# Optimization experiments

Hardware: AMD Instinct MI355X
Metric: run time of the kernel (lower is better)

Reference implementation:

```python
import jax, jax.numpy as jnp
import numpy as np
import math

D_MODEL = 1024
N_HEADS = 16
HEAD_DIM = D_MODEL // N_HEADS
B, S = 4, 4096


def setup_inputs() -> dict:
    key = jax.random.key(0)
    ks = jax.random.split(key, 8)
    # xavier-uniform-ish scale for square DxD matrices
    lim = math.sqrt(6.0 / (D_MODEL + D_MODEL))
    def W(k):
        return jax.random.uniform(k, (D_MODEL, D_MODEL), jnp.float32, -lim, lim)
    return {
        "x": jax.random.normal(ks[0], (B, S, D_MODEL), jnp.float32),
        "fractal_dim": jnp.float32(1.7),
        "Wq": W(ks[1]), "bq": jnp.zeros((D_MODEL,), jnp.float32),
        "Wk": W(ks[2]), "bk": jnp.zeros((D_MODEL,), jnp.float32),
        "Wv": W(ks[3]), "bv": jnp.zeros((D_MODEL,), jnp.float32),
        "Wo": W(ks[4]), "bo": jnp.zeros((D_MODEL,), jnp.float32),
        "alpha": jnp.float32(1.5),
        "frac_scale": jnp.float32(0.5),
    }


def reference(x, fractal_dim, Wq, bq, Wk, bk, Wv, bv, Wo, bo, alpha, frac_scale):
    b, s, d = x.shape
    h, hd = N_HEADS, HEAD_DIM
    residual = x

    adaptive_alpha = alpha + frac_scale * (fractal_dim - 1.5)

    q = (x @ Wq + bq).reshape(b, s, h, hd)
    k = (x @ Wk + bk).reshape(b, s, h, hd)
    v = (x @ Wv + bv).reshape(b, s, h, hd)

    # spectral filter over frequency axis (seq dim)
    freqs = jnp.fft.fftfreq(s).astype(x.dtype)  # [S]
    phase = adaptive_alpha * jnp.arctan(jnp.log(jnp.abs(freqs) + 1e-10))
    filt = jnp.exp(1j * phase)[None, :, None, None]  # [1,S,1,1] complex

    def spectral(t):
        tf = jnp.fft.fft(t, axis=1, norm="ortho") * filt
        return jnp.fft.ifft(tf, axis=1, norm="ortho").real

    q_t, k_t, v_t = spectral(q), spectral(k), spectral(v)

    # per-(token) dot product across head_dim -> logits over heads
    logits = jnp.einsum("bshd,bshd->bsh", q_t, k_t) / math.sqrt(hd)
    w = jax.nn.softmax(logits, axis=-1)  # softmax over heads
    attended = w[..., None] * v_t  # [B,S,H,Hd]

    # final inverse FFT of the (real) attended signal along seq dim
    attended_time = jnp.fft.ifft(attended.astype(jnp.complex64), axis=1, norm="ortho").real

    out = attended_time.reshape(b, s, d) @ Wo + bo
    return out + residual
```

## Files before the change

kernel.cpp:

```cpp
#include <hip/hip_runtime.h>

#define S      4096
#define DM     1024
#define NB     4
#define NH     16
#define HDIM   64
#define MTOT   (NB * S)
#define DS     ((long)DM * S)
#define MH     2304
#define KH     2112
#define KH2    2112
#define MEO    2048

typedef __attribute__((ext_vector_type(8))) short short8;
typedef __attribute__((ext_vector_type(4))) float f32x4;
typedef __attribute__((ext_vector_type(8))) unsigned short u16x8;
typedef __attribute__((ext_vector_type(4))) unsigned short u16x4;

__device__ __forceinline__ unsigned short f2bf(float f) {
  union { float f; unsigned u; } v; v.f = f;
  unsigned r = v.u + 0x7fffu + ((v.u >> 16) & 1u);
  return (unsigned short)(r >> 16);
}
__device__ __forceinline__ float bf2f(short h) {
  union { unsigned u; float f; } v; v.u = ((unsigned)(unsigned short)h) << 16;
  return v.f;
}

#define GLOAD(gp, lp) __builtin_amdgcn_global_load_lds( \
    (const __attribute__((address_space(1))) void*)(gp), \
    (__attribute__((address_space(3))) void*)(lp), 16, 0, 0)

#define SBAR() do { asm volatile("" ::: "memory"); __builtin_amdgcn_s_barrier(); \
                    asm volatile("" ::: "memory"); } while (0)
#define WAITL0() asm volatile("s_waitcnt lgkmcnt(0)" ::: "memory")

#define SWZ(o) ((o) ^ ((((o) >> 7) & 3) << 4))


__global__ void k_tabg(const float* __restrict__ fd, const float* __restrict__ alpha,
                       const float* __restrict__ fsc,
                       float* __restrict__ cos_tab, float* __restrict__ c_arr,
                       float* __restrict__ g) {
  const float twopi = 6.28318530717958647692f;
  float aa = alpha[0] + fsc[0] * (fd[0] - 1.5f);
  int bx = blockIdx.x;
  if (bx < 16) {
    int k = bx * 256 + threadIdx.x;
    cos_tab[k] = cosf(twopi * ((float)k / (float)S));
    int kk = (k <= S / 2) ? k : (S - k);
    float af = (float)kk / (float)S;
    c_arr[k] = cosf(aa * atanf(logf(af + 1e-10f)));
    return;
  }
  __shared__ float sct[S];
  __shared__ float sc[S];
  __shared__ float red[16][17];
  for (int i = threadIdx.x; i < S; i += 256) {
    sct[i] = cosf(twopi * ((float)i / (float)S));
    int kk = (i <= S / 2) ? i : (S - i);
    float af = (float)kk / (float)S;
    sc[i] = cosf(aa * atanf(logf(af + 1e-10f)));
  }
  __syncthreads();
  int jl = threadIdx.x >> 4, r = threadIdx.x & 15;
  int j = (bx - 16) * 16 + jl;
  float acc = 0.f;
#pragma unroll 4
  for (int i = 0; i < 256; ++i) {
    int k = r + 16 * i;
    acc += sc[k] * sct[(j * k) & (S - 1)];
  }
  red[jl][r] = acc;
  __syncthreads();
  if (r == 0) {
    float s = 0.f;
#pragma unroll
    for (int i = 0; i < 16; ++i) s += red[jl][i];
    g[j] = s * (1.f / (float)S);
  }
}

__global__ void k_buildEO(const float* __restrict__ g, short* __restrict__ Ge) {
  long i8 = ((long)blockIdx.x * 256 + threadIdx.x) * 8;
  if (i8 >= (long)MEO * KH2) return;
  int n = (int)(i8 / KH2);
  int m = (int)(i8 % KH2);
  u16x8 ev, ov;
#pragma unroll
  for (int j = 0; j < 8; ++j) {
    int mm = m + j;
    float e, o;
    if (mm == 0)            { e = g[n]; o = 0.f; }
    else if (mm == 2048)    { e = g[(n + 2048) & (S - 1)]; o = 0.f; }
    else if (mm > 2048)     { e = 0.f; o = 0.f; }
    else {
      float a = g[(n - mm) & (S - 1)], b = g[(n + mm) & (S - 1)];
      e = 0.5f * (a + b); o = 0.5f * (a - b);
    }
    ev[j] = f2bf(e); ov[j] = f2bf(o);
  }
  *(u16x8*)(Ge + i8) = ev;
  *(u16x8*)(Ge + (long)MEO * KH2 + i8) = ov;
}

__global__ void k_prep(const float* __restrict__ x, short* __restrict__ uv,
                       const float* __restrict__ W0, const float* __restrict__ W1,
                       const float* __restrict__ W2, const float* __restrict__ W3,
                       short* __restrict__ WT) {
  __shared__ float sh[2 * 64 * 65];
  int bx = blockIdx.x, by = blockIdx.y, bz = blockIdx.z;
  int t = threadIdx.x;
  int r = t >> 4, c4 = (t & 15) * 4;
  if (bx >= 33) {
    float (*tile)[65] = (float(*)[65])sh;
    const float* W = (bz == 0) ? W0 : ((bz == 1) ? W1 : ((bz == 2) ? W2 : W3));
    short* WTo = WT + (size_t)bz * DM * DM;
    int k0 = (bx - 33) * 64, n0 = by * 64;
    const float* ip = W + (long)k0 * DM + n0;
#pragma unroll
    for (int rr = 0; rr < 4; ++rr) {
      float4 v = *(const float4*)(ip + (long)(r + rr * 16) * DM + c4);
      tile[r + rr * 16][c4 + 0] = v.x;
      tile[r + rr * 16][c4 + 1] = v.y;
      tile[r + rr * 16][c4 + 2] = v.z;
      tile[r + rr * 16][c4 + 3] = v.w;
    }
    __syncthreads();
    int k_loc = t & 63, nq = t >> 6;
    short* op = WTo + (long)n0 * DM + k0;
#pragma unroll
    for (int i = 0; i < 16; ++i) {
      int n_loc = nq * 16 + i;
      op[(long)n_loc * DM + k_loc] = (short)f2bf(tile[k_loc][n_loc]);
    }
    return;
  }
  float (*tp)[65] = (float(*)[65])sh;
  float (*tm)[65] = (float(*)[65])(sh + 64 * 65);
  int m0 = bx * 64, d0 = by * 64, b = bz;
#pragma unroll
  for (int rr = 0; rr < 4; ++rr) {
    int m = m0 + r + rr * 16;
    float4 vp = *(const float4*)(x + ((long)(b * S + m)) * DM + d0 + c4);
    int ms = (S - m) & (S - 1);
    float4 vm = *(const float4*)(x + ((long)(b * S + ms)) * DM + d0 + c4);
    tp[r + rr * 16][c4 + 0] = vp.x; tp[r + rr * 16][c4 + 1] = vp.y;
    tp[r + rr * 16][c4 + 2] = vp.z; tp[r + rr * 16][c4 + 3] = vp.w;
    tm[r + rr * 16][c4 + 0] = vm.x; tm[r + rr * 16][c4 + 1] = vm.y;
    tm[r + rr * 16][c4 + 2] = vm.z; tm[r + rr * 16][c4 + 3] = vm.w;
  }
  __syncthreads();
  int m_loc = t & 63, dq = t >> 6;
#pragma unroll
  for (int i = 0; i < 16; ++i) {
    int d_loc = dq * 16 + i;
    int m = m0 + m_loc;
    float P = tp[m_loc][d_loc], M = tm[m_loc][d_loc];
    float u, v;
    if (m == 0 || m == 2048) { u = P; v = 0.f; }
    else if (m > 2048)       { u = 0.f; v = 0.f; }
    else                     { u = P + M; v = P - M; }
    long base = ((long)(b * DM + d0 + d_loc)) * KH2 + m;
    uv[base] = (short)f2bf(u);
    uv[base + (long)4 * DM * KH2] = (short)f2bf(v);
  }
}

__global__ void k_unfold2(const short* __restrict__ AB, const float* __restrict__ g,
                          const short* __restrict__ uv, short* __restrict__ Xs) {
  __shared__ float red[256];
  int bx = blockIdx.x;
  if (bx < 4096) {
    long i8 = ((long)bx * 256 + threadIdx.x) * 8;
    int b = (int)(i8 >> 21);
    long rr = i8 & ((1L << 21) - 1);
    int n = (int)(rr >> 10);
    int d = (int)(rr & (DM - 1));
    u16x8 av = *(const u16x8*)(AB + i8);
    u16x8 bv = *(const u16x8*)(AB + ((long)4 * MEO * DM) + i8);
    u16x8 sv, dv;
#pragma unroll
    for (int j = 0; j < 8; ++j) {
      float A = bf2f((short)av[j]), B = bf2f((short)bv[j]);
      sv[j] = f2bf(A + B);
      dv[j] = f2bf(A - B);
    }
    *(u16x8*)(Xs + ((long)b * S + n) * DM + d) = sv;
    if (n > 0)
      *(u16x8*)(Xs + ((long)b * S + (S - n)) * DM + d) = dv;
  } else {
    int bd = bx - 4096;
    int b = bd >> 10, d = bd & (DM - 1);
    const short* up = uv + ((long)(b * DM + d)) * KH2;
    int t = threadIdx.x;
    float acc = 0.f;
    for (int m = t; m <= 2048; m += 256)
      acc += g[2048 - m] * bf2f(up[m]);
    red[t] = acc;
    __syncthreads();
    for (int sh = 128; sh > 0; sh >>= 1) {
      if (t < sh) red[t] += red[t + sh];
      __syncthreads();
    }
    if (t == 0) Xs[((long)b * S + 2048) * DM + d] = (short)f2bf(red[0]);
  }
}

__global__ void k_logsoft(const short* __restrict__ Q, const short* __restrict__ K,
                          float* __restrict__ w) {
  int idx = blockIdx.x * 16 + (threadIdx.x >> 4);
  int h = threadIdx.x & 15;
  const short* q = Q + (long)idx * DM + h * HDIM;
  const short* k = K + (long)idx * DM + h * HDIM;
  float acc = 0.f;
#pragma unroll
  for (int jj = 0; jj < 8; ++jj) {
    u16x8 qa = *(const u16x8*)(q + jj * 8);
    u16x8 ka = *(const u16x8*)(k + jj * 8);
#pragma unroll
    for (int l = 0; l < 8; ++l) acc += bf2f((short)qa[l]) * bf2f((short)ka[l]);
  }
  acc *= 0.125f;
  float m = acc;
#pragma unroll
  for (int d = 1; d < 16; d <<= 1) m = fmaxf(m, __shfl_xor(m, d, 16));
  float e = expf(acc - m);
  float ssum = e;
#pragma unroll
  for (int d = 1; d < 16; d <<= 1) ssum += __shfl_xor(ssum, d, 16);
  int b = idx >> 12, s = idx & (S - 1);
  w[((long)b * NH + h) * S + s] = e / ssum;
}

__global__ void k_attfoldM2(const short* __restrict__ V, const float* __restrict__ wsm,
                            short* __restrict__ A2t,
                            const float* __restrict__ cos_tab, short* __restrict__ Mc2) {
  int bx = blockIdx.x, by = blockIdx.y, bz = blockIdx.z;
  if (bx >= 33) {
    long lin = (long)(bx - 33) + 38L * (by + 16L * bz);
    long i8 = (lin * 256 + threadIdx.x) * 8;
    if (i8 >= (long)MH * KH) return;
    int n = (int)(i8 / KH);
    int m = (int)(i8 % KH);
    u16x8 mv;
#pragma unroll
    for (int j = 0; j < 8; ++j) {
      int mm = m + j;
      float vv = (mm <= 2048) ? cos_tab[(n * mm) & (S - 1)] * 0.015625f : 0.f;
      mv[j] = f2bf(vv);
    }
    *(u16x8*)(Mc2 + i8) = mv;
    return;
  }
  __shared__ float t1[64][65];
  __shared__ float t2[64][65];
  __shared__ float w1[64], w2[64];
  int m0 = bx * 64, d0 = by * 64, b = bz;
  int t = threadIdx.x;
  int h0 = d0 >> 6;
  if (t < 64) {
    int m = m0 + t;
    const float* wp = wsm + ((long)b * NH + h0) * S;
    w1[t] = wp[m & (S - 1)];
    w2[t] = wp[(S - m) & (S - 1)];
  }
  int r = t >> 4, c4 = (t & 15) * 4;
#pragma unroll
  for (int rr = 0; rr < 4; ++rr) {
    int i = r + rr * 16;
    int m = m0 + i;
    u16x4 a = *(const u16x4*)(V + ((long)(b * S + (m & (S - 1)))) * DM + d0 + c4);
    u16x4 bb = *(const u16x4*)(V + ((long)(b * S + ((S - m) & (S - 1)))) * DM + d0 + c4);
#pragma unroll
    for (int l = 0; l < 4; ++l) {
      t1[i][c4 + l] = bf2f((short)a[l]);
      t2[i][c4 + l] = bf2f((short)bb[l]);
    }
  }
  __syncthreads();
  int i_loc = t & 63, jq = t >> 6;
  int m = m0 + i_loc;
#pragma unroll
  for (int jj = 0; jj < 16; ++jj) {
    int j = jq * 16 + jj;
    float rv;
    if (m == 0 || m == 2048) rv = w1[i_loc] * t1[i_loc][j];
    else if (m < 2048)       rv = w1[i_loc] * t1[i_loc][j] + w2[i_loc] * t2[i_loc][j];
    else                     rv = 0.f;
    A2t[((long)(b * DM + d0 + j)) * KH + m] = (short)f2bf(rv);
  }
}

template <int EPI, int AMIR = 0, int ASEL = 0, int WALK = 0, int MREP = 1>
__global__ __launch_bounds__(512, 2) void gemm8(
    const short* __restrict__ A, const short* __restrict__ Bt,
    short* __restrict__ Cb, short* __restrict__ Cb2, short* __restrict__ Cb3,
    float* __restrict__ Cf,
    const float* __restrict__ bias, const float* __restrict__ bias2,
    const float* __restrict__ bias3,
    const float* __restrict__ bsc, const float* __restrict__ resid,
    int M, int N, int K, long aBatch, long bBatch, long cBatch) {
  __shared__ __align__(16) short SH[65536];
  auto Ab = [&](int buf, int ks) { return SH + (buf * 2 + ks) * 8192; };
  auto Bb = [&](int buf, int ks) { return SH + 32768 + (buf * 2 + ks) * 8192; };

  const int gx = gridDim.x, gy = gridDim.y;
  const int nwg = gx * gy * gridDim.z;
  int lin = blockIdx.x + gx * (blockIdx.y + gy * blockIdx.z);
  int swz = lin;
  if ((nwg & 7) == 0) {
    const int cpx = nwg >> 3;
    swz = (lin & 7) * cpx + (lin >> 3);
  }
  const int NTN = N >> 8;
  const int NTM = M >> 8;
  const int tid = threadIdx.x;
  const int lane = tid & 63;
  const int wid = tid >> 6;
  const int wm = wid >> 2, wn = wid & 3;

  const int o0 = tid * 16, o1 = o0 + 8192;
  const int lo0 = SWZ(o0), lo1 = SWZ(o1);
  const int srow[2] = {lo0 >> 6, lo1 >> 6};
  const int scol[2] = {(lo0 & 63) >> 1, (lo1 & 63) >> 1};

  for (int rep = 0; rep < MREP; ++rep) {
    const int wg = swz + rep * nwg;
    int ntile, mtile, bz;
    if (WALK) {
      mtile = wg % NTM;
      const int rest = wg / NTM;
      ntile = rest % NTN;
      bz = rest / NTN;
    } else {
      ntile = wg % NTN;
      const int rest = wg / NTN;
      mtile = rest % NTM;
      bz = rest / NTM;
    }

    const short* Ag = ASEL ? (A + (long)(bz >> 2) * aBatch) : (A + (long)bz * aBatch);
    const short* Bg = Bt + (long)bz * bBatch;
    const int m0 = mtile << 8, n0 = ntile << 8;

    const short* bA[2];
    const short* bB[2];
#pragma unroll
    for (int j = 0; j < 2; ++j) {
      if (AMIR) {
        int grow = m0 + srow[j];
        int b_ = grow >> 12, s_ = grow & (S - 1);
        int sm = (s_ <= 2048) ? s_ : (4096 - s_);
        bA[j] = Ag + ((long)b_ * MH + sm) * K + scol[j];
      } else {
        bA[j] = Ag + (long)(m0 + srow[j]) * K + scol[j];
      }
      bB[j] = Bg + (long)(n0 + srow[j]) * K + scol[j];
    }

    f32x4 acc[8][4];
#pragma unroll
    for (int i = 0; i < 8; ++i)
#pragma unroll
      for (int j = 0; j < 4; ++j) acc[i][j] = (f32x4){0.f, 0.f, 0.f, 0.f};

    const int NT = K >> 6;
    auto stage = [&](int h) {
      const int tau = h >> 2, q = h & 3;
      const int ks = q >> 1;
      const long k0 = (long)tau * 64 + ks * 32;
      const int dbase = (q & 1) * 65536 + (((tau & 1) << 1) + ks) * 16384;
      const short* b0 = (q & 1) ? bB[0] : bA[0];
      const short* b1 = (q & 1) ? bB[1] : bA[1];
      GLOAD(b0 + k0, (short*)((char*)SH + dbase + o0));
      GLOAD(b1 + k0, (short*)((char*)SH + dbase + o1));
    };

    if (rep > 0) SBAR();
#pragma unroll
    for (int h = 0; h < 7; ++h) stage(h);
    asm volatile("s_waitcnt vmcnt(6)" ::: "memory");
    SBAR();

    short8 bf[4];
    for (int t = 0; t < NT; ++t) {
      const int buf = t & 1;
#pragma unroll
      for (int p = 0; p < 4; ++p) {
        const int ks = p >> 1, mh = p & 1;
        short8 af[4];
        {
          const short* Ah = Ab(buf, ks);
          const int kb = (lane >> 4) * 16;
          const int r0 = wm * 128 + mh * 64 + (lane & 15);
#pragma unroll
          for (int i = 0; i < 4; ++i) {
            int byte = (r0 + i * 16) * 64 + kb;
            byte = SWZ(byte);
            af[i] = *(const short8*)((const char*)Ah + byte);
          }
          if (mh == 0) {
            const short* Bh = Bb(buf, ks);
            const int c0 = wn * 64 + (lane & 15);
#pragma unroll
            for (int j = 0; j < 4; ++j) {
              int byte = (c0 + j * 16) * 64 + kb;
              byte = SWZ(byte);
              bf[j] = *(const short8*)((const char*)Bh + byte);
            }
          }
        }
        { const int h = 4 * t + p + 7; if (h < 4 * NT) stage(h); }
        SBAR();
        WAITL0();
        __builtin_amdgcn_s_setprio(1);
#pragma unroll
        for (int i = 0; i < 4; ++i)
#pragma unroll
          for (int j = 0; j < 4; ++j)
            acc[mh * 4 + i][j] = __builtin_amdgcn_mfma_f32_16x16x32_bf16(
                af[i], bf[j], acc[mh * 4 + i][j], 0, 0, 0);
        __builtin_amdgcn_s_setprio(0);
        if (p == 3) {
          if (t < NT - 2) {
            asm volatile("s_waitcnt vmcnt(6)" ::: "memory");
          } else if (t == NT - 2) {
            asm volatile("s_waitcnt vmcnt(0)" ::: "memory");
          }
        }
        SBAR();
      }
    }

    const int rl = (lane >> 4) << 2;
#pragma unroll
    for (int f = 0; f < 8; ++f) {
      const int rbase = m0 + wm * 128 + f * 16 + rl;
#pragma unroll
      for (int j = 0; j < 4; ++j) {
        const int col = n0 + wn * 64 + j * 16 + (lane & 15);
        f32x4 a = acc[f][j];
        if constexpr (EPI == 0) {
          short* cp = Cb + (long)bz * cBatch;
#pragma unroll
          for (int r = 0; r < 4; ++r)
            cp[(long)(rbase + r) * N + col] = (short)f2bf(a[r]);
        } else if constexpr (EPI == 4) {
          const int pidx = col >> 10;
          const int dcol = col & (DM - 1);
          short* Cp = (pidx == 0) ? Cb : ((pidx == 1) ? Cb2 : Cb3);
          const float* bp = (pidx == 0) ? bias : ((pidx == 1) ? bias2 : bias3);
          const float bi = bp[dcol] * (bsc ? bsc[0] : 1.f);
#pragma unroll
          for (int r = 0; r < 4; ++r)
            Cp[(long)(rbase + r) * DM + dcol] = (short)f2bf(a[r] + bi);
        } else {
          float bi = bias[col];
#pragma unroll
          for (int r = 0; r < 4; ++r) {
            long o = (long)(rbase + r) * N + col;
            Cf[o] = a[r] + bi + resid[o];
          }
        }
      }
    }
  }
}

extern "C" void kernel_launch(void* const* d_in, const int* in_sizes, int n_in,
                              void* d_out, int out_size, void* d_ws, size_t ws_size,
                              hipStream_t stream) {
  const float* x     = (const float*)d_in[0];
  const float* fd    = (const float*)d_in[1];
  const float* Wq    = (const float*)d_in[2];
  const float* bq    = (const float*)d_in[3];
  const float* Wk    = (const float*)d_in[4];
  const float* bk    = (const float*)d_in[5];
  const float* Wv    = (const float*)d_in[6];
  const float* bv    = (const float*)d_in[7];
  const float* Wo    = (const float*)d_in[8];
  const float* bo    = (const float*)d_in[9];
  const float* alpha = (const float*)d_in[10];
  const float* fsc   = (const float*)d_in[11];
  float* out = (float*)d_out;

  char* wp = (char*)d_ws;
  auto alloc = [&](size_t bytes) {
    char* p = wp;
    wp += (bytes + 255) & ~(size_t)255;
    return p;
  };
  float* cos_tab = (float*)alloc(S * 4);
  float* c_arr   = (float*)alloc(S * 4);
  float* g       = (float*)alloc(S * 4);
  float* wsm     = (float*)alloc((size_t)NB * NH * S * 4);
  short* WTcat = (short*)alloc((size_t)4 * DM * DM * 2);
  short* WoT   = WTcat + (size_t)3 * DM * DM;
  short* slotA = (short*)alloc((size_t)NB * DS * 2);
  short* slotB = (short*)alloc((size_t)NB * DS * 2);
  short* slotC = (short*)alloc((size_t)NB * DS * 2);

  short* uv = (short*)d_out;
  short* Qn = (short*)d_out;
  short* Kn = (short*)d_out + (size_t)NB * DS;

  short* Ge  = slotB;
  short* ABout = slotA;
  short* Xs  = slotC;
  short* Vn  = slotA;
  short* Mc2 = slotB;
  short* A2t = (short*)((char*)slotB + 10u * 1024 * 1024);
  short* att_half = slotC;

  dim3 blk(256), blk8(512);

  k_tabg<<<dim3(16 + S / 16), blk, 0, stream>>>(fd, alpha, fsc, cos_tab, c_arr, g);
  k_buildEO<<<dim3((unsigned)((long)MEO * KH2 / 8 / 256)), blk, 0, stream>>>(g, Ge);
  k_prep<<<dim3(49, 16, NB), blk, 0, stream>>>(x, uv, Wq, Wk, Wv, Wo, WTcat);

  dim3 geo(DM / 256, MEO / 256, 8);
  gemm8<0, 0, 1><<<geo, blk8, 0, stream>>>(Ge, uv, ABout, nullptr, nullptr, nullptr,
                                           nullptr, nullptr, nullptr, nullptr, nullptr,
                                           MEO, DM, KH2,
                                           (long)MEO * KH2, (long)DM * KH2, (long)MEO * DM);
  k_unfold2<<<dim3(8192), blk, 0, stream>>>(ABout, g, uv, Xs);

  gemm8<4, 0, 0, 0, 3><<<dim3(256), blk8, 0, stream>>>(
      Xs, WTcat, Qn, Kn, Vn, nullptr, bq, bk, bv, c_arr, nullptr,
      MTOT, 3 * DM, DM, 0, 0, 0);

  k_logsoft<<<dim3(MTOT / 16), blk, 0, stream>>>(Qn, Kn, wsm);
  k_attfoldM2<<<dim3(33 + 38, DM / 64, NB), blk, 0, stream>>>(Vn, wsm, A2t, cos_tab, Mc2);

  dim3 ghalf(DM / 256, MH / 256, NB);
  gemm8<0><<<ghalf, blk8, 0, stream>>>(Mc2, A2t, att_half, nullptr, nullptr, nullptr,
                                       nullptr, nullptr, nullptr, nullptr, nullptr,
                                       MH, DM, KH, 0, (long)DM * KH, (long)MH * DM);

  dim3 gproj(DM / 256, MTOT / 256, 1);
  gemm8<2, 1><<<gproj, blk8, 0, stream>>>(att_half, WoT, nullptr, nullptr, nullptr, out,
                                          bo, nullptr, nullptr, nullptr, x,
                                          MTOT, DM, DM, 0, 0, 0);
}
```

Measured before the change: 389.0 us.

## Switch GEMMs to 128x128 tiles with 256 threads and fold buildEO into prep

Replaces the 256x256-tile, 512-thread GEMM (including its persistent multi-rep variant) with a 128x128-tile, 256-thread GEMM that uses half the shared memory, and relaunches every GEMM with a correspondingly larger grid. The Ge even/odd matrix construction is merged into the k_prep launch as extra blocks, removing one kernel launch. Smaller tiles give more workgroups and better occupancy, at the cost of lower arithmetic intensity per tile and more global traffic.

```diff
diff --git a/kernel.cpp b/kernel.cpp
--- a/kernel.cpp
+++ b/kernel.cpp
@@ -81,36 +81,38 @@
   }
 }
 
-__global__ void k_buildEO(const float* __restrict__ g, short* __restrict__ Ge) {
-  long i8 = ((long)blockIdx.x * 256 + threadIdx.x) * 8;
-  if (i8 >= (long)MEO * KH2) return;
-  int n = (int)(i8 / KH2);
-  int m = (int)(i8 % KH2);
-  u16x8 ev, ov;
-#pragma unroll
-  for (int j = 0; j < 8; ++j) {
-    int mm = m + j;
-    float e, o;
-    if (mm == 0)            { e = g[n]; o = 0.f; }
-    else if (mm == 2048)    { e = g[(n + 2048) & (S - 1)]; o = 0.f; }
-    else if (mm > 2048)     { e = 0.f; o = 0.f; }
-    else {
-      float a = g[(n - mm) & (S - 1)], b = g[(n + mm) & (S - 1)];
-      e = 0.5f * (a + b); o = 0.5f * (a - b);
-    }
-    ev[j] = f2bf(e); ov[j] = f2bf(o);
-  }
-  *(u16x8*)(Ge + i8) = ev;
-  *(u16x8*)(Ge + (long)MEO * KH2 + i8) = ov;
-}
-
 __global__ void k_prep(const float* __restrict__ x, short* __restrict__ uv,
                        const float* __restrict__ W0, const float* __restrict__ W1,
                        const float* __restrict__ W2, const float* __restrict__ W3,
-                       short* __restrict__ WT) {
+                       short* __restrict__ WT,
+                       const float* __restrict__ g, short* __restrict__ Ge) {
   __shared__ float sh[2 * 64 * 65];
   int bx = blockIdx.x, by = blockIdx.y, bz = blockIdx.z;
   int t = threadIdx.x;
+  if (bx >= 49) {
+    long lin = (long)(bx - 49) + 54L * (by + 16L * bz);
+    long i8 = (lin * 256 + t) * 8;
+    if (i8 >= (long)MEO * KH2) return;
+    int n = (int)(i8 / KH2);
+    int m = (int)(i8 % KH2);
+    u16x8 ev, ov;
+#pragma unroll
+    for (int j = 0; j < 8; ++j) {
+      int mm = m + j;
+      float e, o;
+      if (mm == 0)            { e = g[n]; o = 0.f; }
+      else if (mm == 2048)    { e = g[(n + 2048) & (S - 1)]; o = 0.f; }
+      else if (mm > 2048)     { e = 0.f; o = 0.f; }
+      else {
+        float a = g[(n - mm) & (S - 1)], b = g[(n + mm) & (S - 1)];
+        e = 0.5f * (a + b); o = 0.5f * (a - b);
+      }
+      ev[j] = f2bf(e); ov[j] = f2bf(o);
+    }
+    *(u16x8*)(Ge + i8) = ev;
+    *(u16x8*)(Ge + (long)MEO * KH2 + i8) = ov;
+    return;
+  }
   int r = t >> 4, c4 = (t & 15) * 4;
   if (bx >= 33) {
     float (*tile)[65] = (float(*)[65])sh;
@@ -292,8 +294,8 @@
   }
 }
 
-template <int EPI, int AMIR = 0, int ASEL = 0, int WALK = 0, int MREP = 1>
-__global__ __launch_bounds__(512, 2) void gemm8(
+template <int EPI, int AMIR = 0, int ASEL = 0>
+__global__ __launch_bounds__(256, 2) void gemm4(
     const short* __restrict__ A, const short* __restrict__ Bt,
     short* __restrict__ Cb, short* __restrict__ Cb2, short* __restrict__ Cb3,
     float* __restrict__ Cf,
@@ -301,9 +303,9 @@
     const float* __restrict__ bias3,
     const float* __restrict__ bsc, const float* __restrict__ resid,
     int M, int N, int K, long aBatch, long bBatch, long cBatch) {
-  __shared__ __align__(16) short SH[65536];
-  auto Ab = [&](int buf, int ks) { return SH + (buf * 2 + ks) * 8192; };
-  auto Bb = [&](int buf, int ks) { return SH + 32768 + (buf * 2 + ks) * 8192; };
+  __shared__ __align__(16) short SH[32768];
+  auto Ab = [&](int buf, int ks) { return SH + (buf * 2 + ks) * 4096; };
+  auto Bb = [&](int buf, int ks) { return SH + 16384 + (buf * 2 + ks) * 4096; };
 
   const int gx = gridDim.x, gy = gridDim.y;
   const int nwg = gx * gy * gridDim.z;
@@ -313,155 +315,142 @@
     const int cpx = nwg >> 3;
     swz = (lin & 7) * cpx + (lin >> 3);
   }
-  const int NTN = N >> 8;
-  const int NTM = M >> 8;
+  const int NTN = N >> 7;
+  const int NTM = M >> 7;
+  const int ntile = swz % NTN;
+  const int rest = swz / NTN;
+  const int mtile = rest % NTM;
+  const int bz = rest / NTM;
+
+  const short* Ag = ASEL ? (A + (long)(bz >> 2) * aBatch) : (A + (long)bz * aBatch);
+  const short* Bg = Bt + (long)bz * bBatch;
+  const int m0 = mtile << 7, n0 = ntile << 7;
   const int tid = threadIdx.x;
   const int lane = tid & 63;
   const int wid = tid >> 6;
-  const int wm = wid >> 2, wn = wid & 3;
-
-  const int o0 = tid * 16, o1 = o0 + 8192;
+  const int wm = wid >> 1, wn = wid & 1;
+
+  const int o0 = tid * 16, o1 = o0 + 4096;
   const int lo0 = SWZ(o0), lo1 = SWZ(o1);
   const int srow[2] = {lo0 >> 6, lo1 >> 6};
   const int scol[2] = {(lo0 & 63) >> 1, (lo1 & 63) >> 1};
 
-  for (int rep = 0; rep < MREP; ++rep) {
-    const int wg = swz + rep * nwg;
-    int ntile, mtile, bz;
-    if (WALK) {
-      mtile = wg % NTM;
-      const int rest = wg / NTM;
-      ntile = rest % NTN;
-      bz = rest / NTN;
+  const short* bA[2];
+  const short* bB[2];
+#pragma unroll
+  for (int j = 0; j < 2; ++j) {
+    if (AMIR) {
+      int grow = m0 + srow[j];
+      int b_ = grow >> 12, s_ = grow & (S - 1);
+      int sm = (s_ <= 2048) ? s_ : (4096 - s_);
+      bA[j] = Ag + ((long)b_ * MH + sm) * K + scol[j];
     } else {
-      ntile = wg % NTN;
-      const int rest = wg / NTN;
-      mtile = rest % NTM;
-      bz = rest / NTM;
-    }
-
-    const short* Ag = ASEL ? (A + (long)(bz >> 2) * aBatch) : (A + (long)bz * aBatch);
-    const short* Bg = Bt + (long)bz * bBatch;
-    const int m0 = mtile << 8, n0 = ntile << 8;
-
-    const short* bA[2];
-    const short* bB[2];
-#pragma unroll
-    for (int j = 0; j < 2; ++j) {
-      if (AMIR) {
-        int grow = m0 + srow[j];
-        int b_ = grow >> 12, s_ = grow & (S - 1);
-        int sm = (s_ <= 2048) ? s_ : (4096 - s_);
-        bA[j] = Ag + ((long)b_ * MH + sm) * K + scol[j];
-      } else {
-        bA[j] = Ag + (long)(m0 + srow[j]) * K + scol[j];
-      }
-      bB[j] = Bg + (long)(n0 + srow[j]) * K + scol[j];
-    }
-
-    f32x4 acc[8][4];
-#pragma unroll
-    for (int i = 0; i < 8; ++i)
-#pragma unroll
-      for (int j = 0; j < 4; ++j) acc[i][j] = (f32x4){0.f, 0.f, 0.f, 0.f};
-
-    const int NT = K >> 6;
-    auto stage = [&](int h) {
-      const int tau = h >> 2, q = h & 3;
-      const int ks = q >> 1;
-      const long k0 = (long)tau * 64 + ks * 32;
-      const int dbase = (q & 1) * 65536 + (((tau & 1) << 1) + ks) * 16384;
-      const short* b0 = (q & 1) ? bB[0] : bA[0];
-      const short* b1 = (q & 1) ? bB[1] : bA[1];
-      GLOAD(b0 + k0, (short*)((char*)SH + dbase + o0));
-      GLOAD(b1 + k0, (short*)((char*)SH + dbase + o1));
-    };
-
-    if (rep > 0) SBAR();
-#pragma unroll
-    for (int h = 0; h < 7; ++h) stage(h);
-    asm volatile("s_waitcnt vmcnt(6)" ::: "memory");
-    SBAR();
-
-    short8 bf[4];
-    for (int t = 0; t < NT; ++t) {
-      const int buf = t & 1;
-#pragma unroll
-      for (int p = 0; p < 4; ++p) {
-        const int ks = p >> 1, mh = p & 1;
-        short8 af[4];
-        {
-          const short* Ah = Ab(buf, ks);
-          const int kb = (lane >> 4) * 16;
-          const int r0 = wm * 128 + mh * 64 + (lane & 15);
-#pragma unroll
-          for (int i = 0; i < 4; ++i) {
-            int byte = (r0 + i * 16) * 64 + kb;
+      bA[j] = Ag + (long)(m0 + srow[j]) * K + scol[j];
+    }
+    bB[j] = Bg + (long)(n0 + srow[j]) * K + scol[j];
+  }
+
+  f32x4 acc[4][4];
+#pragma unroll
+  for (int i = 0; i < 4; ++i)
+#pragma unroll
+    for (int j = 0; j < 4; ++j) acc[i][j] = (f32x4){0.f, 0.f, 0.f, 0.f};
+
+  const int NT = K >> 6;
+  auto stage = [&](int h) {
+    const int tau = h >> 2, q = h & 3;
+    const int ks = q >> 1;
+    const long k0 = (long)tau * 64 + ks * 32;
+    const int dbase = (q & 1) * 32768 + (((tau & 1) << 1) + ks) * 8192;
+    const short* b0 = (q & 1) ? bB[0] : bA[0];
+    const short* b1 = (q & 1) ? bB[1] : bA[1];
+    GLOAD(b0 + k0, (short*)((char*)SH + dbase + o0));
+    GLOAD(b1 + k0, (short*)((char*)SH + dbase + o1));
+  };
+
+#pragma unroll
+  for (int h = 0; h < 7; ++h) stage(h);
+  asm volatile("s_waitcnt vmcnt(6)" ::: "memory");
+  SBAR();
+
+  short8 bf[4];
+  for (int t = 0; t < NT; ++t) {
+    const int buf = t & 1;
+#pragma unroll
+    for (int p = 0; p < 4; ++p) {
+      const int ks = p >> 1, mh = p & 1;
+      short8 af[2];
+      {
+        const short* Ah = Ab(buf, ks);
+        const int kb = (lane >> 4) * 16;
+        const int r0 = wm * 64 + mh * 32 + (lane & 15);
+#pragma unroll
+        for (int i = 0; i < 2; ++i) {
+          int byte = (r0 + i * 16) * 64 + kb;
+          byte = SWZ(byte);
+          af[i] = *(const short8*)((const char*)Ah + byte);
+        }
+        if (mh == 0) {
+          const short* Bh = Bb(buf, ks);
+          const int c0 = wn * 64 + (lane & 15);
+#pragma unroll
+          for (int j = 0; j < 4; ++j) {
+            int byte = (c0 + j * 16) * 64 + kb;
             byte = SWZ(byte);
-            af[i] = *(const short8*)((const char*)Ah + byte);
-          }
-          if (mh == 0) {
-            const short* Bh = Bb(buf, ks);
-            const int c0 = wn * 64 + (lane & 15);
-#pragma unroll
-            for (int j = 0; j < 4; ++j) {
-              int byte = (c0 + j * 16) * 64 + kb;
-              byte = SWZ(byte);
-              bf[j] = *(const short8*)((const char*)Bh + byte);
-            }
+            bf[j] = *(const short8*)((const char*)Bh + byte);
           }
         }
-        { const int h = 4 * t + p + 7; if (h < 4 * NT) stage(h); }
-        SBAR();
-        WAITL0();
-        __builtin_amdgcn_s_setprio(1);
-#pragma unroll
-        for (int i = 0; i < 4; ++i)
-#pragma unroll
-          for (int j = 0; j < 4; ++j)
-            acc[mh * 4 + i][j] = __builtin_amdgcn_mfma_f32_16x16x32_bf16(
-                af[i], bf[j], acc[mh * 4 + i][j], 0, 0, 0);
-        __builtin_amdgcn_s_setprio(0);
-        if (p == 3) {
-          if (t < NT - 2) {
-            asm volatile("s_waitcnt vmcnt(6)" ::: "memory");
-          } else if (t == NT - 2) {
-            asm volatile("s_waitcnt vmcnt(0)" ::: "memory");
-          }
+      }
+      { const int h = 4 * t + p + 7; if (h < 4 * NT) stage(h); }
+      SBAR();
+      WAITL0();
+      __builtin_amdgcn_s_setprio(1);
+#pragma unroll
+      for (int i = 0; i < 2; ++i)
+#pragma unroll
+        for (int j = 0; j < 4; ++j)
+          acc[mh * 2 + i][j] = __builtin_amdgcn_mfma_f32_16x16x32_bf16(
+              af[i], bf[j], acc[mh * 2 + i][j], 0, 0, 0);
+      __builtin_amdgcn_s_setprio(0);
+      if (p == 3) {
+        if (t < NT - 2) {
+          asm volatile("s_waitcnt vmcnt(6)" ::: "memory");
+        } else if (t == NT - 2) {
+          asm volatile("s_waitcnt vmcnt(0)" ::: "memory");
         }
-        SBAR();
       }
-    }
-
-    const int rl = (lane >> 4) << 2;
-#pragma unroll
-    for (int f = 0; f < 8; ++f) {
-      const int rbase = m0 + wm * 128 + f * 16 + rl;
-#pragma unroll
-      for (int j = 0; j < 4; ++j) {
-        const int col = n0 + wn * 64 + j * 16 + (lane & 15);
-        f32x4 a = acc[f][j];
-        if constexpr (EPI == 0) {
-          short* cp = Cb + (long)bz * cBatch;
-#pragma unroll
-          for (int r = 0; r < 4; ++r)
-            cp[(long)(rbase + r) * N + col] = (short)f2bf(a[r]);
-        } else if constexpr (EPI == 4) {
-          const int pidx = col >> 10;
-          const int dcol = col & (DM - 1);
-          short* Cp = (pidx == 0) ? Cb : ((pidx == 1) ? Cb2 : Cb3);
-          const float* bp = (pidx == 0) ? bias : ((pidx == 1) ? bias2 : bias3);
-          const float bi = bp[dcol] * (bsc ? bsc[0] : 1.f);
-#pragma unroll
-          for (int r = 0; r < 4; ++r)
-            Cp[(long)(rbase + r) * DM + dcol] = (short)f2bf(a[r] + bi);
-        } else {
-          float bi = bias[col];
-#pragma unroll
-          for (int r = 0; r < 4; ++r) {
-            long o = (long)(rbase + r) * N + col;
-            Cf[o] = a[r] + bi + resid[o];
-          }
+      SBAR();
+    }
+  }
+
+  const int rl = (lane >> 4) << 2;
+#pragma unroll
+  for (int f = 0; f < 4; ++f) {
+    const int rbase = m0 + wm * 64 + f * 16 + rl;
+#pragma unroll
+    for (int j = 0; j < 4; ++j) {
+      const int col = n0 + wn * 64 + j * 16 + (lane & 15);
+      f32x4 a = acc[f][j];
+      if constexpr (EPI == 0) {
+        short* cp = Cb + (long)bz * cBatch;
+#pragma unroll
+        for (int r = 0; r < 4; ++r)
+          cp[(long)(rbase + r) * N + col] = (short)f2bf(a[r]);
+      } else if constexpr (EPI == 4) {
+        const int pidx = col >> 10;
+        const int dcol = col & (DM - 1);
+        short* Cp = (pidx == 0) ? Cb : ((pidx == 1) ? Cb2 : Cb3);
+        const float* bp = (pidx == 0) ? bias : ((pidx == 1) ? bias2 : bias3);
+        const float bi = bp[dcol] * (bsc ? bsc[0] : 1.f);
+#pragma unroll
+        for (int r = 0; r < 4; ++r)
+          Cp[(long)(rbase + r) * DM + dcol] = (short)f2bf(a[r] + bi);
+      } else {
+        float bi = bias[col];
+#pragma unroll
+        for (int r = 0; r < 4; ++r) {
+          long o = (long)(rbase + r) * N + col;
+          Cf[o] = a[r] + bi + resid[o];
         }
       }
     }
@@ -513,33 +502,33 @@
   short* A2t = (short*)((char*)slotB + 10u * 1024 * 1024);
   short* att_half = slotC;
 
-  dim3 blk(256), blk8(512);
+  dim3 blk(256);
 
   k_tabg<<<dim3(16 + S / 16), blk, 0, stream>>>(fd, alpha, fsc, cos_tab, c_arr, g);
-  k_buildEO<<<dim3((unsigned)((long)MEO * KH2 / 8 / 256)), blk, 0, stream>>>(g, Ge);
-  k_prep<<<dim3(49, 16, NB), blk, 0, stream>>>(x, uv, Wq, Wk, Wv, Wo, WTcat);
-
-  dim3 geo(DM / 256, MEO / 256, 8);
-  gemm8<0, 0, 1><<<geo, blk8, 0, stream>>>(Ge, uv, ABout, nullptr, nullptr, nullptr,
-                                           nullptr, nullptr, nullptr, nullptr, nullptr,
-                                           MEO, DM, KH2,
-                                           (long)MEO * KH2, (long)DM * KH2, (long)MEO * DM);
+  k_prep<<<dim3(49 + 54, 16, NB), blk, 0, stream>>>(x, uv, Wq, Wk, Wv, Wo, WTcat, g, Ge);
+
+  dim3 geo(DM / 128, MEO / 128, 8);
+  gemm4<0, 0, 1><<<geo, blk, 0, stream>>>(Ge, uv, ABout, nullptr, nullptr, nullptr,
+                                          nullptr, nullptr, nullptr, nullptr, nullptr,
+                                          MEO, DM, KH2,
+                                          (long)MEO * KH2, (long)DM * KH2, (long)MEO * DM);
   k_unfold2<<<dim3(8192), blk, 0, stream>>>(ABout, g, uv, Xs);
 
-  gemm8<4, 0, 0, 0, 3><<<dim3(256), blk8, 0, stream>>>(
-      Xs, WTcat, Qn, Kn, Vn, nullptr, bq, bk, bv, c_arr, nullptr,
-      MTOT, 3 * DM, DM, 0, 0, 0);
+  dim3 gqkv(3 * DM / 128, MTOT / 128, 1);
+  gemm4<4><<<gqkv, blk, 0, stream>>>(Xs, WTcat, Qn, Kn, Vn, nullptr,
+                                     bq, bk, bv, c_arr, nullptr,
+                                     MTOT, 3 * DM, DM, 0, 0, 0);
 
   k_logsoft<<<dim3(MTOT / 16), blk, 0, stream>>>(Qn, Kn, wsm);
   k_attfoldM2<<<dim3(33 + 38, DM / 64, NB), blk, 0, stream>>>(Vn, wsm, A2t, cos_tab, Mc2);
 
-  dim3 ghalf(DM / 256, MH / 256, NB);
-  gemm8<0><<<ghalf, blk8, 0, stream>>>(Mc2, A2t, att_half, nullptr, nullptr, nullptr,
-                                       nullptr, nullptr, nullptr, nullptr, nullptr,
-                                       MH, DM, KH, 0, (long)DM * KH, (long)MH * DM);
-
-  dim3 gproj(DM / 256, MTOT / 256, 1);
-  gemm8<2, 1><<<gproj, blk8, 0, stream>>>(att_half, WoT, nullptr, nullptr, nullptr, out,
-                                          bo, nullptr, nullptr, nullptr, x,
-                                          MTOT, DM, DM, 0, 0, 0);
-}
+  dim3 ghalf(DM / 128, MH / 128, NB);
+  gemm4<0><<<ghalf, blk, 0, stream>>>(Mc2, A2t, att_half, nullptr, nullptr, nullptr,
+                                      nullptr, nullptr, nullptr, nullptr, nullptr,
+                                      MH, DM, KH, 0, (long)DM * KH, (long)MH * DM);
+
+  dim3 gproj(DM / 128, MTOT / 128, 1);
+  gemm4<2, 1><<<gproj, blk, 0, stream>>>(att_half, WoT, nullptr, nullptr, nullptr, out,
+                                         bo, nullptr, nullptr, nullptr, x,
+                                         MTOT, DM, DM, 0, 0, 0);
+}
```

Result: slower. 417.8 us (+7.4%).
